# Optimization experiments

Hardware: AMD Instinct MI355X
Metric: run time of the kernel (lower is better)

Reference implementation:

```python
import jax, jax.numpy as jnp
import numpy as np

N_NODES = 100000
N_EDGES = 3200000
N_FEAT = 500
N_HID = 256
N_CLASS = 40


def spmm(edge_row, edge_col, edge_val, x, num_nodes):
    # out[i] = sum_{e: row[e]==i} val[e] * x[col[e]]
    msgs = edge_val[:, None] * x[edge_col]          # [E, F] gather + scale
    return jax.ops.segment_sum(msgs, edge_row, num_segments=num_nodes)


def setup_inputs() -> dict:
    key = jax.random.key(0)
    k1, k2, k3, k4, k5, k6, k7, k8 = jax.random.split(key, 8)
    features = jax.random.normal(k1, (N_NODES, N_FEAT), dtype=jnp.float32)
    edge_row = jax.random.randint(k2, (N_EDGES,), 0, N_NODES, dtype=jnp.int32)
    edge_col = jax.random.randint(k3, (N_EDGES,), 0, N_NODES, dtype=jnp.int32)
    edge_val = jax.random.uniform(k4, (N_EDGES,), dtype=jnp.float32)
    # Xavier-uniform linear weights, zero biases (as in reset_parameters)
    lim1 = float(np.sqrt(6.0 / (N_FEAT + N_HID)))
    W1 = jax.random.uniform(k5, (N_FEAT, N_HID), minval=-lim1, maxval=lim1, dtype=jnp.float32)
    b1 = jnp.zeros((N_HID,), dtype=jnp.float32)
    lim2 = float(np.sqrt(6.0 / (N_HID + N_CLASS)))
    W2 = jax.random.uniform(k6, (N_HID, N_CLASS), minval=-lim2, maxval=lim2, dtype=jnp.float32)
    b2 = jnp.zeros((N_CLASS,), dtype=jnp.float32)
    return {
        "features": features,
        "edge_row": edge_row,
        "edge_col": edge_col,
        "edge_val": edge_val,
        "W1": W1, "b1": b1, "W2": W2, "b2": b2,
    }


def reference(features, edge_row, edge_col, edge_val, W1, b1, W2, b2):
    # Layer 1: linear -> spmm -> relu   (eval mode: dropout is identity)
    h = features @ W1 + b1                          # [N, nhid]
    h = spmm(edge_row, edge_col, edge_val, h, N_NODES)
    h = jax.nn.relu(h)
    # Layer 2: linear -> spmm
    o = h @ W2 + b2                                 # [N, nclass]
    o = spmm(edge_row, edge_col, edge_val, o, N_NODES)
    return jax.nn.log_softmax(o, axis=1)
```

## Files before the change

kernel.cpp:

```cpp
#include <hip/hip_runtime.h>
#include <hip/hip_bf16.h>
#include <math.h>

#define N_NODES 100000
#define N_FEAT 500
#define N_HID 256
#define N_CLASS 40

typedef float f32x4 __attribute__((ext_vector_type(4)));
typedef float f32x2 __attribute__((ext_vector_type(2)));
typedef int i32x4 __attribute__((ext_vector_type(4)));
typedef unsigned int u32x4 __attribute__((ext_vector_type(4)));
typedef short short8 __attribute__((ext_vector_type(8)));
typedef unsigned short u16x8 __attribute__((ext_vector_type(8)));

__device__ __forceinline__ float b2f(unsigned short u) {
  union { unsigned int i; float f; } c; c.i = ((unsigned int)u) << 16; return c.f;
}
__device__ __forceinline__ unsigned short f2bu(float x) {
  __hip_bfloat16 b = __float2bfloat16(x);
  union { __hip_bfloat16 b; unsigned short u; } c; c.b = b; return c.u;
}
__device__ __forceinline__ float decode_val(unsigned int p) {
  union { unsigned int i; float f; } c; c.i = (p & 0x7FFFu) << 17; return c.f;
}
__device__ __forceinline__ unsigned char f2fp8(float x) {
  return (unsigned char)(__builtin_amdgcn_cvt_pk_fp8_f32(x, x, 0, false) & 0xFF);
}
__device__ __forceinline__ void gload_lds16(const void* gptr, void* lptr) {
  __builtin_amdgcn_global_load_lds(
      (const __attribute__((address_space(1))) unsigned int*)gptr,
      (__attribute__((address_space(3))) unsigned int*)lptr, 16, 0, 0);
}

__global__ __launch_bounds__(256) void prep_kernel(
    const float* __restrict__ W1, unsigned short* __restrict__ Bsw,
    const int* __restrict__ er, const int* __restrict__ ec,
    const float* __restrict__ ev, int* __restrict__ cnt,
    unsigned int* __restrict__ cvps, int E) {
  if (blockIdx.x < 64) {
    int t = blockIdx.x * 256 + threadIdx.x;
    int col = t >> 6, ch = t & 63;
    int g = ch >> 3, c = ch & 7;
    int c_src = c ^ (col & 7);
    int k = g * 64 + c_src * 8;
    u16x8 o;
#pragma unroll
    for (int j = 0; j < 8; j++) {
      int kk = k + j;
      o[j] = (kk < N_FEAT) ? f2bu(W1[(size_t)kk * N_HID + col]) : (unsigned short)0;
    }
    *(u16x8*)(Bsw + (size_t)col * 512 + g * 64 + c * 8) = o;
  }
  int nv = E >> 2;
  int t = blockIdx.x * 256 + threadIdx.x;
  int nthr = gridDim.x * 256;
  const i32x4* er4 = (const i32x4*)er;
  const i32x4* ec4 = (const i32x4*)ec;
  const f32x4* ev4 = (const f32x4*)ev;
  for (int i = t; i < nv; i += nthr) {
    i32x4 r = __builtin_nontemporal_load(&er4[i]);
    i32x4 c = __builtin_nontemporal_load(&ec4[i]);
    f32x4 v = __builtin_nontemporal_load(&ev4[i]);
    atomicAdd(&cnt[r.x], 1);
    atomicAdd(&cnt[r.y], 1);
    atomicAdd(&cnt[r.z], 1);
    atomicAdd(&cnt[r.w], 1);
    u32x4 pk;
    pk.x = ((unsigned int)c.x << 15) | ((unsigned int)f2bu(v.x) >> 1);
    pk.y = ((unsigned int)c.y << 15) | ((unsigned int)f2bu(v.y) >> 1);
    pk.z = ((unsigned int)c.z << 15) | ((unsigned int)f2bu(v.z) >> 1);
    pk.w = ((unsigned int)c.w << 15) | ((unsigned int)f2bu(v.w) >> 1);
    __builtin_nontemporal_store(pk, (u32x4*)(cvps + 4 * (size_t)i));
  }
  int tail = nv << 2;
  if (blockIdx.x == 0 && threadIdx.x < E - tail) {
    int i = tail + threadIdx.x;
    atomicAdd(&cnt[er[i]], 1);
    cvps[i] = ((unsigned int)ec[i] << 15) | ((unsigned int)f2bu(ev[i]) >> 1);
  }
}

__global__ __launch_bounds__(256) void gemm1_mfma(
    const float* __restrict__ A, const unsigned short* __restrict__ Bsw,
    const float* __restrict__ b1, unsigned char* __restrict__ H, int M) {
  __shared__ __align__(16) char smem[36864];
  char* sA = smem;
  char* sB = smem + 4096;
  int tid = threadIdx.x;
  int lane = tid & 63, w = tid >> 6;
  int wc = w;
  int bm = blockIdx.x * 32;

  f32x4 acc[2][4];
#pragma unroll
  for (int m = 0; m < 2; m++)
#pragma unroll
    for (int n = 0; n < 4; n++) acc[m][n] = (f32x4)0.f;

  for (int s = 0; s < 8; s++) {
    int k0 = s * 64;
#pragma unroll
    for (int i = 0; i < 2; i++) {
      int f4 = i * 256 + tid;
      int row = f4 >> 4, cidx = f4 & 15;
      int grow = bm + row;
      int k = k0 + cidx * 4;
      float4 v = make_float4(0.f, 0.f, 0.f, 0.f);
      if (grow < M && k < N_FEAT) v = *(const float4*)(A + (size_t)grow * N_FEAT + k);
      ushort4 u;
      u.x = f2bu(v.x); u.y = f2bu(v.y); u.z = f2bu(v.z); u.w = f2bu(v.w);
      int chunk = cidx >> 1, sub = cidx & 1;
      int byte = row * 128 + (((chunk ^ (row & 7))) << 4) + (sub << 3);
      *(ushort4*)(sA + byte) = u;
    }
#pragma unroll
    for (int j = 0; j < 8; j++) {
      int base = j * 4096 + w * 1024;
      int L = base + lane * 16;
      int col = L >> 7, c = (L >> 4) & 7;
      const char* g = (const char*)Bsw + (size_t)col * 1024 + s * 128 + c * 16;
      gload_lds16(g, sB + base);
    }
    __syncthreads();
#pragma unroll
    for (int kk = 0; kk < 2; kk++) {
      int cw = kk * 4 + (lane >> 4);
      short8 af[2], bg[4];
#pragma unroll
      for (int m = 0; m < 2; m++) {
        int ar = m * 16 + (lane & 15);
        af[m] = *(const short8*)(sA + ar * 128 + ((cw ^ (ar & 7)) << 4));
      }
#pragma unroll
      for (int n = 0; n < 4; n++) {
        int bc = wc * 64 + n * 16 + (lane & 15);
        bg[n] = *(const short8*)(sB + bc * 128 + ((cw ^ (bc & 7)) << 4));
      }
#pragma unroll
      for (int m = 0; m < 2; m++)
#pragma unroll
        for (int n = 0; n < 4; n++)
          acc[m][n] = __builtin_amdgcn_mfma_f32_16x16x32_bf16(af[m], bg[n], acc[m][n], 0, 0, 0);
    }
    __syncthreads();
  }

  float bias[4];
#pragma unroll
  for (int n = 0; n < 4; n++) bias[n] = b1[wc * 64 + n * 16 + (lane & 15)];
#pragma unroll
  for (int m = 0; m < 2; m++) {
#pragma unroll
    for (int r = 0; r < 4; r++) {
      int row = bm + m * 16 + ((lane >> 4) << 2) + r;
      if (row < M) {
#pragma unroll
        for (int n = 0; n < 4; n++) {
          int col = wc * 64 + n * 16 + (lane & 15);
          H[(size_t)row * N_HID + col] = f2fp8(acc[m][n][r] + bias[n]);
        }
      }
    }
  }
}

__global__ __launch_bounds__(1024) void scan1_kernel(
    int* __restrict__ cnt, int* __restrict__ bsum, int n) {
  __shared__ int wsum[16];
  int tid = threadIdx.x, lane = tid & 63, wid = tid >> 6;
  int i = blockIdx.x * 1024 + tid;
  int v = (i < n) ? cnt[i] : 0;
  int x = v;
#pragma unroll
  for (int off = 1; off < 64; off <<= 1) {
    int t = __shfl_up(x, off);
    if (lane >= off) x += t;
  }
  if (lane == 63) wsum[wid] = x;
  __syncthreads();
  if (tid < 16) {
    int ws = wsum[tid];
#pragma unroll
    for (int off = 1; off < 16; off <<= 1) {
      int t = __shfl_up(ws, off);
      if (tid >= off) ws += t;
    }
    wsum[tid] = ws;
  }
  __syncthreads();
  int excl = (wid ? wsum[wid - 1] : 0) + x - v;
  if (i < n) cnt[i] = excl;
  if (tid == 0) bsum[blockIdx.x] = wsum[15];
}

__global__ __launch_bounds__(64) void scan2_kernel(
    int* __restrict__ bsum, int* __restrict__ row_ptr, int nb, int n) {
  int lane = threadIdx.x;
  int carry = 0;
  for (int base = 0; base < nb; base += 64) {
    int i = base + lane;
    int v = (i < nb) ? bsum[i] : 0;
    int x = v;
#pragma unroll
    for (int off = 1; off < 64; off <<= 1) {
      int t = __shfl_up(x, off);
      if (lane >= off) x += t;
    }
    if (i < nb) bsum[i] = carry + x - v;
    carry += __shfl(x, 63);
  }
  if (lane == 0) row_ptr[n] = carry;
}

__global__ __launch_bounds__(256) void scan3_kernel(
    int* __restrict__ cnt, const int* __restrict__ bsum,
    int* __restrict__ row_ptr, int n) {
  int i = blockIdx.x * 256 + threadIdx.x;
  if (i >= n) return;
  int v = cnt[i] + bsum[i >> 10];
  cnt[i] = v;
  row_ptr[i] = v;
}

__global__ __launch_bounds__(256) void scatter_kernel(
    const int* __restrict__ er, const unsigned int* __restrict__ cvps,
    int* __restrict__ cursor, unsigned int* __restrict__ cvp, int E) {
  int s = blockIdx.x & 3;
  int g = blockIdx.x >> 2;
  int ngrp = gridDim.x >> 2;
  int nv = E >> 2;
  const i32x4* er4 = (const i32x4*)er;
  const u32x4* cv4 = (const u32x4*)cvps;
  for (int i = g * 256 + threadIdx.x; i < nv; i += ngrp * 256) {
    i32x4 r = __builtin_nontemporal_load(&er4[i]);
    u32x4 p = __builtin_nontemporal_load(&cv4[i]);
    if (((r.x >> 9) & 3) == s) cvp[atomicAdd(&cursor[r.x], 1)] = p.x;
    if (((r.y >> 9) & 3) == s) cvp[atomicAdd(&cursor[r.y], 1)] = p.y;
    if (((r.z >> 9) & 3) == s) cvp[atomicAdd(&cursor[r.z], 1)] = p.z;
    if (((r.w >> 9) & 3) == s) cvp[atomicAdd(&cursor[r.w], 1)] = p.w;
  }
  int tail = nv << 2;
  if (blockIdx.x == 0 && threadIdx.x < E - tail) {
    int i = tail + threadIdx.x;
    cvp[atomicAdd(&cursor[er[i]], 1)] = cvps[i];
  }
}

__global__ __launch_bounds__(256) void spmm_fp8(
    const int* __restrict__ row_ptr, const unsigned int* __restrict__ cvp,
    const unsigned char* __restrict__ X, unsigned short* __restrict__ Y, int M) {
  int wave = (blockIdx.x * 256 + threadIdx.x) >> 6;
  int lane = threadIdx.x & 63;
  if (wave >= M) return;
  int start = row_ptr[wave], end = row_ptr[wave + 1];
  int qf = lane >> 4, fl = lane & 15;
  f32x4 a0 = (f32x4)0.f, a1 = (f32x4)0.f, a2 = (f32x4)0.f, a3 = (f32x4)0.f;
  const unsigned char* Xf = X + fl * 16;
  unsigned int pcur;
  {
    int ei = start + qf;
    pcur = (ei < end) ? cvp[ei] : 0u;
  }
#pragma unroll 2
  for (int e = start; e < end; e += 4) {
    int en = e + 4 + qf;
    unsigned int pnext = (en < end) ? cvp[en] : 0u;
    float val = decode_val(pcur);
    size_t col = (size_t)(pcur >> 15);
    u32x4 d = *(const u32x4*)(Xf + col * N_HID);
    f32x2 f0 = __builtin_amdgcn_cvt_pk_f32_fp8(d.x, false);
    f32x2 f1 = __builtin_amdgcn_cvt_pk_f32_fp8(d.x, true);
    f32x2 f2 = __builtin_amdgcn_cvt_pk_f32_fp8(d.y, false);
    f32x2 f3 = __builtin_amdgcn_cvt_pk_f32_fp8(d.y, true);
    f32x2 f4 = __builtin_amdgcn_cvt_pk_f32_fp8(d.z, false);
    f32x2 f5 = __builtin_amdgcn_cvt_pk_f32_fp8(d.z, true);
    f32x2 f6 = __builtin_amdgcn_cvt_pk_f32_fp8(d.w, false);
    f32x2 f7 = __builtin_amdgcn_cvt_pk_f32_fp8(d.w, true);
    a0.x = fmaf(val, f0.x, a0.x); a0.y = fmaf(val, f0.y, a0.y);
    a0.z = fmaf(val, f1.x, a0.z); a0.w = fmaf(val, f1.y, a0.w);
    a1.x = fmaf(val, f2.x, a1.x); a1.y = fmaf(val, f2.y, a1.y);
    a1.z = fmaf(val, f3.x, a1.z); a1.w = fmaf(val, f3.y, a1.w);
    a2.x = fmaf(val, f4.x, a2.x); a2.y = fmaf(val, f4.y, a2.y);
    a2.z = fmaf(val, f5.x, a2.z); a2.w = fmaf(val, f5.y, a2.w);
    a3.x = fmaf(val, f6.x, a3.x); a3.y = fmaf(val, f6.y, a3.y);
    a3.z = fmaf(val, f7.x, a3.z); a3.w = fmaf(val, f7.y, a3.w);
    pcur = pnext;
  }
#define RED2(v) v += __shfl_xor(v, 16); v += __shfl_xor(v, 32);
  RED2(a0.x) RED2(a0.y) RED2(a0.z) RED2(a0.w)
  RED2(a1.x) RED2(a1.y) RED2(a1.z) RED2(a1.w)
  RED2(a2.x) RED2(a2.y) RED2(a2.z) RED2(a2.w)
  RED2(a3.x) RED2(a3.y) RED2(a3.z) RED2(a3.w)
#undef RED2
  if (qf == 0) {
    u16x8 o;
    o[0] = f2bu(fmaxf(a0.x, 0.f)); o[1] = f2bu(fmaxf(a0.y, 0.f));
    o[2] = f2bu(fmaxf(a0.z, 0.f)); o[3] = f2bu(fmaxf(a0.w, 0.f));
    o[4] = f2bu(fmaxf(a1.x, 0.f)); o[5] = f2bu(fmaxf(a1.y, 0.f));
    o[6] = f2bu(fmaxf(a1.z, 0.f)); o[7] = f2bu(fmaxf(a1.w, 0.f));
    *(u16x8*)(Y + (size_t)wave * N_HID + fl * 16) = o;
    o[0] = f2bu(fmaxf(a2.x, 0.f)); o[1] = f2bu(fmaxf(a2.y, 0.f));
    o[2] = f2bu(fmaxf(a2.z, 0.f)); o[3] = f2bu(fmaxf(a2.w, 0.f));
    o[4] = f2bu(fmaxf(a3.x, 0.f)); o[5] = f2bu(fmaxf(a3.y, 0.f));
    o[6] = f2bu(fmaxf(a3.z, 0.f)); o[7] = f2bu(fmaxf(a3.w, 0.f));
    *(u16x8*)(Y + (size_t)wave * N_HID + fl * 16 + 8) = o;
  }
}

__global__ __launch_bounds__(256) void gemm2_kernel(
    const unsigned short* __restrict__ H, const float* __restrict__ W2,
    const float* __restrict__ b2, unsigned short* __restrict__ O, int M) {
  __shared__ float Ws[N_HID * N_CLASS];
  __shared__ float sb2[N_CLASS];
  int tid = threadIdx.x;
  for (int i = tid; i < N_HID * N_CLASS; i += 256) Ws[i] = W2[i];
  if (tid < N_CLASS) sb2[tid] = b2[tid];
  __syncthreads();
  int r0 = (blockIdx.x * 256 + tid) * 2;
  if (r0 >= M) return;
  int r1 = r0 + 1;
  bool has1 = r1 < M;
  float acc0[N_CLASS], acc1[N_CLASS];
#pragma unroll
  for (int n = 0; n < N_CLASS; n++) { acc0[n] = sb2[n]; acc1[n] = sb2[n]; }
  const unsigned short* h0 = H + (size_t)r0 * N_HID;
  const unsigned short* h1 = H + (size_t)(has1 ? r1 : r0) * N_HID;
  for (int k0 = 0; k0 < N_HID; k0 += 8) {
    u16x8 va = *(const u16x8*)(h0 + k0);
    u16x8 vb = *(const u16x8*)(h1 + k0);
#pragma unroll
    for (int j = 0; j < 8; j++) {
      float a0 = b2f(va[j]), a1 = b2f(vb[j]);
      const float* wrow = &Ws[(k0 + j) * N_CLASS];
#pragma unroll
      for (int n = 0; n < N_CLASS; n++) {
        float wv = wrow[n];
        acc0[n] = fmaf(a0, wv, acc0[n]);
        acc1[n] = fmaf(a1, wv, acc1[n]);
      }
    }
  }
  unsigned short* o0 = O + (size_t)r0 * N_CLASS;
#pragma unroll
  for (int n = 0; n < N_CLASS; n += 4) {
    ushort4 p;
    p.x = f2bu(acc0[n]); p.y = f2bu(acc0[n + 1]);
    p.z = f2bu(acc0[n + 2]); p.w = f2bu(acc0[n + 3]);
    *(ushort4*)(o0 + n) = p;
  }
  if (has1) {
    unsigned short* o1 = O + (size_t)r1 * N_CLASS;
#pragma unroll
    for (int n = 0; n < N_CLASS; n += 4) {
      ushort4 p;
      p.x = f2bu(acc1[n]); p.y = f2bu(acc1[n + 1]);
      p.z = f2bu(acc1[n + 2]); p.w = f2bu(acc1[n + 3]);
      *(ushort4*)(o1 + n) = p;
    }
  }
}

__global__ __launch_bounds__(256) void spmm_csr_40_lsm(
    const int* __restrict__ row_ptr, const unsigned int* __restrict__ cvp,
    const unsigned short* __restrict__ X, float* __restrict__ Out, int M) {
  int wave = (blockIdx.x * 256 + threadIdx.x) >> 6;
  int lane = threadIdx.x & 63;
  if (wave >= M) return;
  int start = row_ptr[wave], end = row_ptr[wave + 1];
  bool act = lane < N_CLASS;
  int ln = act ? lane : 0;
  const unsigned short* Xc = X + ln;
  float acc = 0.f;
  int e = start;
  for (; e + 4 <= end; e += 4) {
    unsigned int p0 = cvp[e], p1 = cvp[e + 1], p2 = cvp[e + 2], p3 = cvp[e + 3];
    unsigned short x0 = Xc[(size_t)(p0 >> 15) * N_CLASS];
    unsigned short x1 = Xc[(size_t)(p1 >> 15) * N_CLASS];
    unsigned short x2 = Xc[(size_t)(p2 >> 15) * N_CLASS];
    unsigned short x3 = Xc[(size_t)(p3 >> 15) * N_CLASS];
    acc = fmaf(decode_val(p0), b2f(x0), acc);
    acc = fmaf(decode_val(p1), b2f(x1), acc);
    acc = fmaf(decode_val(p2), b2f(x2), acc);
    acc = fmaf(decode_val(p3), b2f(x3), acc);
  }
  for (; e < end; e++) {
    unsigned int p0 = cvp[e];
    acc = fmaf(decode_val(p0), b2f(Xc[(size_t)(p0 >> 15) * N_CLASS]), acc);
  }
  float mv = act ? acc : -INFINITY;
#pragma unroll
  for (int off = 32; off; off >>= 1) mv = fmaxf(mv, __shfl_xor(mv, off));
  float ex = act ? expf(acc - mv) : 0.f;
  float s = ex;
#pragma unroll
  for (int off = 32; off; off >>= 1) s += __shfl_xor(s, off);
  float lse = mv + logf(s);
  if (act) Out[(size_t)wave * N_CLASS + lane] = acc - lse;
}

extern "C" void kernel_launch(void* const* d_in, const int* in_sizes, int n_in,
                              void* d_out, int out_size, void* d_ws, size_t ws_size,
                              hipStream_t stream) {
  const float* feat = (const float*)d_in[0];
  const int* er     = (const int*)d_in[1];
  const int* ec     = (const int*)d_in[2];
  const float* ev   = (const float*)d_in[3];
  const float* W1   = (const float*)d_in[4];
  const float* b1   = (const float*)d_in[5];
  const float* W2   = (const float*)d_in[6];
  const float* b2   = (const float*)d_in[7];
  float* out = (float*)d_out;
  const int M = N_NODES;
  const int E = in_sizes[1];

  char* ws = (char*)d_ws;
  unsigned char* h      = (unsigned char*)(ws);
  unsigned short* hpost = (unsigned short*)(ws + 25600000);
  unsigned short* o     = (unsigned short*)(ws + 76800000);
  int* row_ptr          = (int*)(ws + 84800000);
  int* cursor           = (int*)(ws + 85200016);
  int* bsum             = (int*)(ws + 85600016);
  unsigned int* cvp     = (unsigned int*)(ws + 85600528);
  unsigned int* cvps    = (unsigned int*)(ws + 98400528);
  unsigned short* W1Tsw = (unsigned short*)(ws + 111200528);

  const int NB1 = (M + 1023) / 1024;

  (void)hipMemsetAsync(cursor, 0, (size_t)M * sizeof(int), stream);
  prep_kernel<<<1024, 256, 0, stream>>>(W1, W1Tsw, er, ec, ev, cursor, cvps, E);
  scan1_kernel<<<NB1, 1024, 0, stream>>>(cursor, bsum, M);
  scan2_kernel<<<1, 64, 0, stream>>>(bsum, row_ptr, NB1, M);
  scan3_kernel<<<(M + 255) / 256, 256, 0, stream>>>(cursor, bsum, row_ptr, M);
  scatter_kernel<<<2048, 256, 0, stream>>>(er, cvps, cursor, cvp, E);
  gemm1_mfma<<<(M + 31) / 32, 256, 0, stream>>>(feat, W1Tsw, b1, h, M);
  spmm_fp8<<<(M + 3) / 4, 256, 0, stream>>>(row_ptr, cvp, h, hpost, M);
  gemm2_kernel<<<(M + 511) / 512, 256, 0, stream>>>(hpost, W2, b2, o, M);
  spmm_csr_40_lsm<<<(M + 3) / 4, 256, 0, stream>>>(row_ptr, cvp, o, out, M);
}
```

Measured before the change: 650.3 us.

## Double-buffer gemm1 with async LDS loads and 64-row tiles

```diff
diff --git a/kernel.cpp b/kernel.cpp
--- a/kernel.cpp
+++ b/kernel.cpp
@@ -6,6 +6,7 @@
 #define N_FEAT 500
 #define N_HID 256
 #define N_CLASS 40
+#define NT1 16
 
 typedef float f32x4 __attribute__((ext_vector_type(4)));
 typedef float f32x2 __attribute__((ext_vector_type(2)));
@@ -40,17 +41,16 @@
     unsigned int* __restrict__ cvps, int E) {
   if (blockIdx.x < 64) {
     int t = blockIdx.x * 256 + threadIdx.x;
-    int col = t >> 6, ch = t & 63;
-    int g = ch >> 3, c = ch & 7;
-    int c_src = c ^ (col & 7);
-    int k = g * 64 + c_src * 8;
+    int col = t >> 6, rem = t & 63;
+    int s = rem >> 2, c16 = rem & 3;
+    int k_src = s * 32 + (c16 ^ (col & 3)) * 8;
     u16x8 o;
 #pragma unroll
     for (int j = 0; j < 8; j++) {
-      int kk = k + j;
+      int kk = k_src + j;
       o[j] = (kk < N_FEAT) ? f2bu(W1[(size_t)kk * N_HID + col]) : (unsigned short)0;
     }
-    *(u16x8*)(Bsw + (size_t)col * 512 + g * 64 + c * 8) = o;
+    *(u16x8*)(Bsw + (size_t)col * 512 + s * 32 + c16 * 8) = o;
   }
   int nv = E >> 2;
   int t = blockIdx.x * 256 + threadIdx.x;
@@ -84,73 +84,97 @@
 __global__ __launch_bounds__(256) void gemm1_mfma(
     const float* __restrict__ A, const unsigned short* __restrict__ Bsw,
     const float* __restrict__ b1, unsigned char* __restrict__ H, int M) {
-  __shared__ __align__(16) char smem[36864];
-  char* sA = smem;
-  char* sB = smem + 4096;
+  __shared__ __align__(16) char smem[49152];
   int tid = threadIdx.x;
   int lane = tid & 63, w = tid >> 6;
   int wc = w;
-  int bm = blockIdx.x * 32;
-
-  f32x4 acc[2][4];
-#pragma unroll
-  for (int m = 0; m < 2; m++)
+  int bm = blockIdx.x * 64;
+
+  f32x4 acc[4][4];
+#pragma unroll
+  for (int m = 0; m < 4; m++)
 #pragma unroll
     for (int n = 0; n < 4; n++) acc[m][n] = (f32x4)0.f;
 
-  for (int s = 0; s < 8; s++) {
-    int k0 = s * 64;
+  auto stageA = [&](int buf, int s) {
+    int k0 = s * 32;
+    char* dst = smem + buf * 8192;
 #pragma unroll
     for (int i = 0; i < 2; i++) {
-      int f4 = i * 256 + tid;
-      int row = f4 >> 4, cidx = f4 & 15;
+      int base = i * 4096 + w * 1024;
+      int L = base + lane * 16;
+      int row = L >> 7;
+      int c16 = (L >> 4) & 7;
+      int c32 = c16 >> 1, sub = c16 & 1;
+      int c32s = c32 ^ (row & 3);
+      int k = k0 + c32s * 8 + sub * 4;
       int grow = bm + row;
-      int k = k0 + cidx * 4;
-      float4 v = make_float4(0.f, 0.f, 0.f, 0.f);
-      if (grow < M && k < N_FEAT) v = *(const float4*)(A + (size_t)grow * N_FEAT + k);
-      ushort4 u;
-      u.x = f2bu(v.x); u.y = f2bu(v.y); u.z = f2bu(v.z); u.w = f2bu(v.w);
-      int chunk = cidx >> 1, sub = cidx & 1;
-      int byte = row * 128 + (((chunk ^ (row & 7))) << 4) + (sub << 3);
-      *(ushort4*)(sA + byte) = u;
-    }
-#pragma unroll
-    for (int j = 0; j < 8; j++) {
+      const float* src = (grow < M && k < N_FEAT)
+                             ? A + (size_t)grow * N_FEAT + k
+                             : A;
+      gload_lds16(src, dst + base);
+    }
+  };
+  auto stageB = [&](int buf, int s) {
+    char* dst = smem + 16384 + buf * 16384;
+#pragma unroll
+    for (int j = 0; j < 4; j++) {
       int base = j * 4096 + w * 1024;
       int L = base + lane * 16;
-      int col = L >> 7, c = (L >> 4) & 7;
-      const char* g = (const char*)Bsw + (size_t)col * 1024 + s * 128 + c * 16;
-      gload_lds16(g, sB + base);
-    }
+      int col = L >> 6;
+      int c16 = (L >> 4) & 3;
+      const char* g = (const char*)Bsw + (size_t)col * 1024 + s * 64 + c16 * 16;
+      gload_lds16(g, dst + base);
+    }
+  };
+  auto compute = [&](int buf) {
+    const char* sA = smem + buf * 8192;
+    const char* sB = smem + 16384 + buf * 16384;
+    int cw = lane >> 4;
+    int lr = lane & 15;
+    short8 af[4], bg[4];
+#pragma unroll
+    for (int m = 0; m < 4; m++) {
+      int ar = m * 16 + lr;
+      const f32x4* p = (const f32x4*)(sA + ar * 128 + ((cw ^ (ar & 3)) << 5));
+      f32x4 lo = p[0];
+      f32x4 hi = p[1];
+      u16x8 t;
+      t[0] = f2bu(lo.x); t[1] = f2bu(lo.y); t[2] = f2bu(lo.z); t[3] = f2bu(lo.w);
+      t[4] = f2bu(hi.x); t[5] = f2bu(hi.y); t[6] = f2bu(hi.z); t[7] = f2bu(hi.w);
+      union { u16x8 u; short8 s; } cv; cv.u = t;
+      af[m] = cv.s;
+    }
+#pragma unroll
+    for (int n = 0; n < 4; n++) {
+      int bc = wc * 64 + n * 16 + lr;
+      bg[n] = *(const short8*)(sB + bc * 64 + ((cw ^ (bc & 3)) << 4));
+    }
+#pragma unroll
+    for (int m = 0; m < 4; m++)
+#pragma unroll
+      for (int n = 0; n < 4; n++)
+        acc[m][n] = __builtin_amdgcn_mfma_f32_16x16x32_bf16(af[m], bg[n], acc[m][n], 0, 0, 0);
+  };
+
+  stageA(0, 0);
+  stageB(0, 0);
+  __syncthreads();
+  int cur = 0;
+  for (int s = 0; s < NT1 - 1; s++) {
+    stageA(cur ^ 1, s + 1);
+    stageB(cur ^ 1, s + 1);
+    compute(cur);
     __syncthreads();
-#pragma unroll
-    for (int kk = 0; kk < 2; kk++) {
-      int cw = kk * 4 + (lane >> 4);
-      short8 af[2], bg[4];
-#pragma unroll
-      for (int m = 0; m < 2; m++) {
-        int ar = m * 16 + (lane & 15);
-        af[m] = *(const short8*)(sA + ar * 128 + ((cw ^ (ar & 7)) << 4));
-      }
-#pragma unroll
-      for (int n = 0; n < 4; n++) {
-        int bc = wc * 64 + n * 16 + (lane & 15);
-        bg[n] = *(const short8*)(sB + bc * 128 + ((cw ^ (bc & 7)) << 4));
-      }
-#pragma unroll
-      for (int m = 0; m < 2; m++)
-#pragma unroll
-        for (int n = 0; n < 4; n++)
-          acc[m][n] = __builtin_amdgcn_mfma_f32_16x16x32_bf16(af[m], bg[n], acc[m][n], 0, 0, 0);
-    }
-    __syncthreads();
-  }
+    cur ^= 1;
+  }
+  compute(cur);
 
   float bias[4];
 #pragma unroll
   for (int n = 0; n < 4; n++) bias[n] = b1[wc * 64 + n * 16 + (lane & 15)];
 #pragma unroll
-  for (int m = 0; m < 2; m++) {
+  for (int m = 0; m < 4; m++) {
 #pragma unroll
     for (int r = 0; r < 4; r++) {
       int row = bm + m * 16 + ((lane >> 4) << 2) + r;
@@ -433,7 +457,7 @@
   scan2_kernel<<<1, 64, 0, stream>>>(bsum, row_ptr, NB1, M);
   scan3_kernel<<<(M + 255) / 256, 256, 0, stream>>>(cursor, bsum, row_ptr, M);
   scatter_kernel<<<2048, 256, 0, stream>>>(er, cvps, cursor, cvp, E);
-  gemm1_mfma<<<(M + 31) / 32, 256, 0, stream>>>(feat, W1Tsw, b1, h, M);
+  gemm1_mfma<<<(M + 63) / 64, 256, 0, stream>>>(feat, W1Tsw, b1, h, M);
   spmm_fp8<<<(M + 3) / 4, 256, 0, stream>>>(row_ptr, cvp, h, hpost, M);
   gemm2_kernel<<<(M + 511) / 512, 256, 0, stream>>>(hpost, W2, b2, o, M);
   spmm_csr_40_lsm<<<(M + 3) / 4, 256, 0, stream>>>(row_ptr, cvp, o, out, M);
```

Result: no change. 638.6 us (-1.8%).
